# Performance work log

Measured on AMD Instinct MI355X. Metric: run time of the kernel, lower is better.

Reference implementation:

```python
import jax, jax.numpy as jnp
import numpy as np

HID = 64

def setup_inputs() -> dict:
    key = jax.random.key(0)
    ks = jax.random.split(key, 20)
    N, E, IN = 20000, 100000, 16
    s = 0.05
    return {
        "nfeat": jax.random.normal(ks[0], (N, IN), dtype=jnp.float32),
        "efeat": jax.random.normal(ks[1], (E, 5), dtype=jnp.float32),
        "src": jax.random.randint(ks[2], (E,), 0, N),
        "dst": jax.random.randint(ks[3], (E,), 0, N),
        "lin0_w": jax.random.normal(ks[4], (IN, HID)) * s,
        "lin0_b": jax.random.normal(ks[5], (HID,)) * s,
        "e1_w": jax.random.normal(ks[6], (5, 128)) * s,
        "e1_b": jax.random.normal(ks[7], (128,)) * s,
        "e2_w": jax.random.normal(ks[8], (128, HID * HID)) * s,
        "e2_b": jax.random.normal(ks[9], (HID * HID,)) * s,
        "conv_bias": jax.random.normal(ks[10], (HID,)) * s,
        "gru_w_ih": jax.random.normal(ks[11], (HID, 3 * HID)) * s,
        "gru_w_hh": jax.random.normal(ks[12], (HID, 3 * HID)) * s,
        "gru_b_ih": jax.random.normal(ks[13], (3 * HID,)) * s,
        "gru_b_hh": jax.random.normal(ks[14], (3 * HID,)) * s,
        "lstm_w_ih": jax.random.normal(ks[15], (2 * HID, 4 * HID)) * s,
        "lstm_w_hh": jax.random.normal(ks[16], (HID, 4 * HID)) * s,
        "lstm_b_ih": jax.random.normal(ks[17], (4 * HID,)) * s,
        "lstm_b_hh": jax.random.normal(ks[18], (4 * HID,)) * s,
    }


def _forward(nfeat, efeat, src, dst, lin0_w, lin0_b, e1_w, e1_b, e2_w, e2_b,
             conv_bias, gru_w_ih, gru_w_hh, gru_b_ih, gru_b_hh,
             lstm_w_ih, lstm_w_hh, lstm_b_ih, lstm_b_hh):
    N = nfeat.shape[0]
    E = efeat.shape[0]
    # lin0 + relu
    out = jax.nn.relu(nfeat @ lin0_w + lin0_b)          # [N, H]
    h = out                                             # GRU hidden state
    # edge MLP -> per-edge weight matrix [E, H, H] (in, out); efeat is fixed across rounds
    w_e = (jax.nn.relu(efeat @ e1_w + e1_b) @ e2_w + e2_b).reshape(E, HID, HID)
    # mean-aggregation denominator (in-degree, clamped like DGL mean over nonempty)
    deg = jax.ops.segment_sum(jnp.ones((E,), out.dtype), dst, num_segments=N)
    denom = jnp.maximum(deg, 1.0)[:, None]
    for _ in range(3):
        msg = jnp.einsum('ei,eio->eo', out[src], w_e)   # edge-conditioned matmul
        agg = jax.ops.segment_sum(msg, dst, num_segments=N) / denom
        m = jax.nn.relu(agg + conv_bias)                # NNConv output + relu
        # GRU cell (torch gate order: r, z, n)
        gi = m @ gru_w_ih + gru_b_ih
        gh = h @ gru_w_hh + gru_b_hh
        ir, iz, inn = jnp.split(gi, 3, axis=-1)
        hr, hz, hn = jnp.split(gh, 3, axis=-1)
        r = jax.nn.sigmoid(ir + hr)
        z = jax.nn.sigmoid(iz + hz)
        n = jnp.tanh(inn + r * hn)
        h = (1.0 - z) * n + z * h
        out = h
    # Set2Set pooling (single graph), LSTM gate order: i, f, g, o
    q_star = jnp.zeros((1, 2 * HID), out.dtype)
    hl = jnp.zeros((1, HID), out.dtype)
    cl = jnp.zeros((1, HID), out.dtype)
    for _ in range(3):
        gates = q_star @ lstm_w_ih + lstm_b_ih + hl @ lstm_w_hh + lstm_b_hh
        i_g, f_g, g_g, o_g = jnp.split(gates, 4, axis=-1)
        cl = jax.nn.sigmoid(f_g) * cl + jax.nn.sigmoid(i_g) * jnp.tanh(g_g)
        hl = jax.nn.sigmoid(o_g) * jnp.tanh(cl)
        q = hl                                          # [1, H]
        e = jnp.sum(out * q, axis=-1)                   # [N]
        alpha = jax.nn.softmax(e)
        readout = jnp.sum(alpha[:, None] * out, axis=0, keepdims=True)  # [1, H]
        q_star = jnp.concatenate([q, readout], axis=1)
    return q_star, out


def reference(nfeat, efeat, src, dst, lin0_w, lin0_b, e1_w, e1_b, e2_w, e2_b,
              conv_bias, gru_w_ih, gru_w_hh, gru_b_ih, gru_b_hh,
              lstm_w_ih, lstm_w_hh, lstm_b_ih, lstm_b_hh):
    return _forward(nfeat, efeat, src, dst, lin0_w, lin0_b, e1_w, e1_b, e2_w,
                    e2_b, conv_bias, gru_w_ih, gru_w_hh, gru_b_ih, gru_b_hh,
                    lstm_w_ih, lstm_w_hh, lstm_b_ih, lstm_b_hh)
```

## Files before the change

kernel.cpp:

```cpp
#include <hip/hip_runtime.h>

#define NN 20000
#define NE 100000
#define EPAD 100096
#define INF 16
#define HID 64

typedef __attribute__((ext_vector_type(8))) short short8;
typedef __attribute__((ext_vector_type(4))) float f32x4;

#define QS   0
#define SHL  128
#define SCL  192
#define SQ   256
#define SSW  324
#define SRD  384

__device__ inline float bf2f(unsigned short u) {
    union { unsigned u32; float f; } c; c.u32 = ((unsigned)u) << 16; return c.f;
}
__device__ inline unsigned short f2b(float f) {
    union { float f; unsigned u; } c; c.f = f;
    unsigned u = c.u;
    unsigned r = u + 0x7fffu + ((u >> 16) & 1u);
    return (unsigned short)(r >> 16);
}
__device__ inline float sigm(float x) { return 1.f / (1.f + expf(-x)); }
__device__ inline short8 s8zero() {
    short8 v;
    #pragma unroll
    for (int z = 0; z < 8; ++z) v[z] = 0;
    return v;
}
__device__ inline void gload_lds16(const void* g, void* l) {
    __builtin_amdgcn_global_load_lds(
        (const __attribute__((address_space(1))) unsigned*)g,
        (__attribute__((address_space(3))) unsigned*)l, 16, 0, 0);
}

__global__ void k_sentinel(float* out) { out[0] = 12345.0f; }

__global__ __launch_bounds__(256) void k_lin0(const float* __restrict__ nfeat,
        const float* __restrict__ w, const float* __restrict__ b,
        float* __restrict__ X, unsigned short* __restrict__ Xb) {
    int t = blockIdx.x * 256 + threadIdx.x;
    int n = t >> 6, o = t & 63;
    float acc = b[o];
    #pragma unroll
    for (int i = 0; i < INF; ++i) acc += nfeat[n * INF + i] * w[i * HID + o];
    float v = fmaxf(acc, 0.f);
    X[t] = v;
    Xb[t] = f2b(v);
}

__global__ void k_count(const int* __restrict__ dst, int* __restrict__ cnt, int E) {
    int e = blockIdx.x * blockDim.x + threadIdx.x;
    if (e < E) atomicAdd(&cnt[dst[e]], 1);
}

__global__ void k_scan(const int* __restrict__ cnt, int* __restrict__ istart) {
    __shared__ int ps[1024];
    int t = threadIdx.x;
    const int CH = (NN + 1023) / 1024;
    int lo = t * CH, hi = (lo + CH < NN) ? lo + CH : NN;
    if (lo > NN) lo = NN;
    if (hi < lo) hi = lo;
    int s = 0;
    for (int i = lo; i < hi; ++i) s += cnt[i];
    ps[t] = s;
    __syncthreads();
    for (int off = 1; off < 1024; off <<= 1) {
        int v = (t >= off) ? ps[t - off] : 0;
        __syncthreads();
        ps[t] += v;
        __syncthreads();
    }
    int run = ps[t] - s;
    for (int i = lo; i < hi; ++i) { istart[i] = run; run += cnt[i]; }
    if (t == 1023) istart[NN] = run;
}

__global__ void k_scatter(const int* __restrict__ src, const int* __restrict__ dst,
        const int* __restrict__ istart, int* __restrict__ cnt2,
        int* __restrict__ ssrc, int* __restrict__ sdst, int* __restrict__ spos, int E) {
    int e = blockIdx.x * blockDim.x + threadIdx.x;
    if (e >= E) return;
    int d = dst[e];
    int p = istart[d] + atomicAdd(&cnt2[d], 1);
    ssrc[p] = src[e];
    sdst[p] = d;
    spos[e] = p;
}

__global__ __launch_bounds__(256) void k_e1(const float* __restrict__ efeat,
        const float* __restrict__ w, const float* __restrict__ b,
        const int* __restrict__ spos, unsigned short* __restrict__ h1b) {
    int t = blockIdx.x * 256 + threadIdx.x;
    int e = t >> 7, k = t & 127;
    float acc = b[k];
    #pragma unroll
    for (int i = 0; i < 5; ++i) acc += efeat[e * 5 + i] * w[i * 128 + k];
    h1b[(size_t)spos[e] * 128 + k] = f2b(fmaxf(acc, 0.f));
}

__global__ __launch_bounds__(256) void k_tr(const float* __restrict__ w2,
        unsigned short* __restrict__ w2t) {
    __shared__ float t[128][65];
    int tid = threadIdx.x;
    int og0 = blockIdx.x * 64;
    for (int v = tid; v < 2048; v += 256) {
        int k = v >> 4, c4 = (v & 15) << 2;
        float4 val = *reinterpret_cast<const float4*>(&w2[(size_t)k * 4096 + og0 + c4]);
        t[k][c4 + 0] = val.x; t[k][c4 + 1] = val.y;
        t[k][c4 + 2] = val.z; t[k][c4 + 3] = val.w;
    }
    __syncthreads();
    int ogl = tid >> 2;
    int k0 = (tid & 3) * 32;
    unsigned short buf[32];
    #pragma unroll
    for (int j = 0; j < 32; ++j) buf[j] = f2b(t[k0 + j][ogl]);
    size_t base = (size_t)(og0 + ogl) * 128;
    #pragma unroll
    for (int q = 0; q < 4; ++q) {
        int s = (tid & 3) * 4 + q;
        int pos = (s ^ (ogl & 7)) * 8;
        short8 pv;
        #pragma unroll
        for (int z = 0; z < 8; ++z) pv[z] = buf[q * 8 + z];
        *reinterpret_cast<short8*>(&w2t[base + pos]) = pv;
    }
}

__global__ void k_prep(const float* __restrict__ e2b, unsigned short* __restrict__ b2t) {
    int t = blockIdx.x * 256 + threadIdx.x;
    int o = t >> 6, i = t & 63;
    b2t[o * 64 + i] = f2b(e2b[i * 64 + o]);
}

__global__ __launch_bounds__(256, 4) void k_msg(
        const unsigned short* __restrict__ Xb,
        const unsigned short* __restrict__ h1b,
        const unsigned short* __restrict__ w2t,
        const unsigned short* __restrict__ b2t,
        const int* __restrict__ ssrc, const int* __restrict__ sdst,
        const int* __restrict__ istart, float* __restrict__ agg) {
    __shared__ __align__(16) char smem[35328];
    unsigned short* xeb = (unsigned short*)(smem + 16384);
    int* sdst_s         = (int*)(smem + 34816);
    const int tid = threadIdx.x;
    const int e0 = blockIdx.x * 128;
    const int y  = blockIdx.y;
    const int w = tid >> 6, l = tid & 63;
    const int wo_l = (w >> 1) * 16;
    const int weh  = (w & 1) * 64;
    const int l15 = l & 15, lh = l >> 4;

    for (int v = tid; v < 1024; v += 256) {
        int row = v >> 3, c8 = (v & 7) << 3;
        int ee = e0 + row;
        short8 val = s8zero();
        if (ee < NE)
            val = *reinterpret_cast<const short8*>(&Xb[(size_t)ssrc[ee] * 64 + c8]);
        *reinterpret_cast<short8*>(&xeb[row * 72 + c8]) = val;
    }
    if (tid < 128) {
        int ee = e0 + tid;
        sdst_s[tid] = (ee < NE) ? sdst[ee] : NN;
    }

    {
        const char* g0 = (const char*)w2t + (size_t)y * 8192;
        gload_lds16(g0 + w * 2048 + l * 16, smem + w * 2048);
        gload_lds16(g0 + w * 2048 + 1024 + l * 16, smem + w * 2048 + 1024);
    }

    short8 bfr[4][4];
    #pragma unroll
    for (int ef = 0; ef < 4; ++ef) {
        const unsigned short* hp = &h1b[(size_t)(e0 + weh + ef * 16 + l15) * 128 + lh * 8];
        #pragma unroll
        for (int ks = 0; ks < 4; ++ks)
            bfr[ef][ks] = *reinterpret_cast<const short8*>(hp + ks * 32);
    }

    f32x4 acc[4];
    #pragma unroll
    for (int ef = 0; ef < 4; ++ef) acc[ef] = f32x4{0.f, 0.f, 0.f, 0.f};
    const f32x4 zero = f32x4{0.f, 0.f, 0.f, 0.f};

    __syncthreads();

    const int r = wo_l + l15;
    const int sw = r & 7;
    int cur = 0;
    #pragma unroll 1
    for (int i = 0; i < 64; ++i) {
        if (i < 63) {
            const char* g = (const char*)w2t + (size_t)(i + 1) * 16384 + (size_t)y * 8192;
            char* dbase = smem + (cur ^ 1) * 8192;
            gload_lds16(g + w * 2048 + l * 16, dbase + w * 2048);
            gload_lds16(g + w * 2048 + 1024 + l * 16, dbase + w * 2048 + 1024);
        }
        float xv[4];
        #pragma unroll
        for (int ef = 0; ef < 4; ++ef)
            xv[ef] = bf2f(xeb[(weh + ef * 16 + l15) * 72 + i]);

        const unsigned short* rb = (const unsigned short*)(smem + cur * 8192) + r * 128;
        short8 a0 = *reinterpret_cast<const short8*>(&rb[((0 + lh) ^ sw) << 3]);
        short8 a1 = *reinterpret_cast<const short8*>(&rb[((4 + lh) ^ sw) << 3]);
        short8 a2 = *reinterpret_cast<const short8*>(&rb[((8 + lh) ^ sw) << 3]);
        short8 a3 = *reinterpret_cast<const short8*>(&rb[((12 + lh) ^ sw) << 3]);
        #pragma unroll
        for (int ef = 0; ef < 4; ++ef) {
            f32x4 t = __builtin_amdgcn_mfma_f32_16x16x32_bf16(a0, bfr[ef][0], zero, 0, 0, 0);
            t = __builtin_amdgcn_mfma_f32_16x16x32_bf16(a1, bfr[ef][1], t, 0, 0, 0);
            t = __builtin_amdgcn_mfma_f32_16x16x32_bf16(a2, bfr[ef][2], t, 0, 0, 0);
            t = __builtin_amdgcn_mfma_f32_16x16x32_bf16(a3, bfr[ef][3], t, 0, 0, 0);
            #pragma unroll
            for (int rr = 0; rr < 4; ++rr) acc[ef][rr] += xv[ef] * t[rr];
        }
        __syncthreads();
        cur ^= 1;
    }

    {
        const unsigned short* bp = &b2t[(y * 32 + r) * 64 + lh * 8];
        short8 ba0 = *reinterpret_cast<const short8*>(bp);
        short8 ba1 = *reinterpret_cast<const short8*>(bp + 32);
        #pragma unroll
        for (int ef = 0; ef < 4; ++ef) {
            int e = e0 + weh + ef * 16 + l15;
            int es = (e < NE) ? ssrc[e] : 0;
            const unsigned short* xp = &Xb[(size_t)es * 64 + lh * 8];
            short8 x0 = *reinterpret_cast<const short8*>(xp);
            short8 x1 = *reinterpret_cast<const short8*>(xp + 32);
            f32x4 tb = __builtin_amdgcn_mfma_f32_16x16x32_bf16(ba0, x0, zero, 0, 0, 0);
            tb = __builtin_amdgcn_mfma_f32_16x16x32_bf16(ba1, x1, tb, 0, 0, 0);
            #pragma unroll
            for (int rr = 0; rr < 4; ++rr) acc[ef][rr] += tb[rr];
        }
    }

    __syncthreads();
    float* msgL = (float*)smem;
    #pragma unroll
    for (int ef = 0; ef < 4; ++ef)
        #pragma unroll
        for (int rr = 0; rr < 4; ++rr)
            msgL[(weh + ef * 16 + l15) * 33 + (wo_l + lh * 4 + rr)] = acc[ef][rr];
    __syncthreads();

    if (tid < 128) {
        int o = tid & 31, win = tid >> 5;
        int base = win << 5;
        int lo = e0 + base, hi = lo + 32;
        int cn = -1; float s = 0.f;
        for (int e2 = base; e2 < base + 32; ++e2) {
            int n = sdst_s[e2];
            if (n != cn) {
                if (cn >= 0 && cn < NN) {
                    int st = istart[cn], en = istart[cn + 1];
                    if (st >= lo && en <= hi) agg[(size_t)cn * 64 + y * 32 + o] = s;
                    else atomicAdd(&agg[(size_t)cn * 64 + y * 32 + o], s);
                }
                cn = n; s = 0.f;
            }
            s += msgL[e2 * 33 + o];
        }
        if (cn >= 0 && cn < NN) {
            int st = istart[cn], en = istart[cn + 1];
            if (st >= lo && en <= hi) agg[(size_t)cn * 64 + y * 32 + o] = s;
            else atomicAdd(&agg[(size_t)cn * 64 + y * 32 + o], s);
        }
    }
}

__global__ __launch_bounds__(256) void k_gru(const float* __restrict__ agg,
        const int* __restrict__ istart, const float* __restrict__ cbias,
        const float* __restrict__ wih, const float* __restrict__ whh,
        const float* __restrict__ bih, const float* __restrict__ bhh,
        float* __restrict__ X, unsigned short* __restrict__ Xb) {
    __shared__ float ms[16][65], hs[16][65];
    int tid = threadIdx.x;
    int l = tid & 63, g = tid >> 6;
    int nb = blockIdx.x * 16;
    for (int v = tid; v < 1024; v += 256) {
        int row = v >> 6, c = v & 63;
        int n = nb + row;
        float dv = fmaxf((float)(istart[n + 1] - istart[n]), 1.f);
        ms[row][c] = fmaxf(agg[(size_t)n * 64 + c] / dv + cbias[c], 0.f);
        hs[row][c] = X[(size_t)n * 64 + c];
    }
    __syncthreads();
    float gr[4], gz[4], gn[4], hr[4], hz[4], hn[4];
    float b0 = bih[l], b1 = bih[64 + l], b2 = bih[128 + l];
    float c0 = bhh[l], c1 = bhh[64 + l], c2 = bhh[128 + l];
    #pragma unroll
    for (int j = 0; j < 4; ++j) {
        gr[j] = b0; gz[j] = b1; gn[j] = b2;
        hr[j] = c0; hz[j] = c1; hn[j] = c2;
    }
    #pragma unroll 4
    for (int i = 0; i < 64; ++i) {
        float wr = wih[i * 192 + l], wz = wih[i * 192 + 64 + l], wn = wih[i * 192 + 128 + l];
        float vr = whh[i * 192 + l], vz = whh[i * 192 + 64 + l], vn = whh[i * 192 + 128 + l];
        #pragma unroll
        for (int j = 0; j < 4; ++j) {
            float mi = ms[g * 4 + j][i], hi = hs[g * 4 + j][i];
            gr[j] += mi * wr; gz[j] += mi * wz; gn[j] += mi * wn;
            hr[j] += hi * vr; hz[j] += hi * vz; hn[j] += hi * vn;
        }
    }
    #pragma unroll
    for (int j = 0; j < 4; ++j) {
        int n = nb + g * 4 + j;
        float h = hs[g * 4 + j][l];
        float r = sigm(gr[j] + hr[j]);
        float z = sigm(gz[j] + hz[j]);
        float nn2 = tanhf(gn[j] + r * hn[j]);
        float newh = (1.f - z) * nn2 + z * h;
        X[(size_t)n * 64 + l] = newh;
        Xb[(size_t)n * 64 + l] = f2b(newh);
    }
}

__global__ void k_lstm(const float* __restrict__ wih, const float* __restrict__ whh,
        const float* __restrict__ bih, const float* __restrict__ bhh,
        float* __restrict__ scal, int it) {
    __shared__ float qs[128];
    __shared__ float g[256];
    int t = threadIdx.x;
    if (t < 128) {
        float v = 0.f;
        if (it > 0)
            v = (t < 64) ? scal[SQ + t]
                         : scal[SRD + (it - 1) * 64 + (t - 64)] / scal[SSW + (it - 1)];
        qs[t] = v;
    }
    __syncthreads();
    float acc = bih[t] + bhh[t];
    for (int i = 0; i < 128; ++i) acc += qs[i] * wih[i * 256 + t];
    for (int i = 0; i < 64; ++i)  acc += scal[SHL + i] * whh[i * 256 + t];
    g[t] = acc;
    __syncthreads();
    if (t < 64) {
        float ig = sigm(g[t]), fg = sigm(g[64 + t]);
        float gg = tanhf(g[128 + t]), og = sigm(g[192 + t]);
        float c = fg * scal[SCL + t] + ig * gg;
        float h = og * tanhf(c);
        scal[SCL + t] = c; scal[SHL + t] = h; scal[SQ + t] = h;
    }
}

__global__ __launch_bounds__(256) void k_pool(const float* __restrict__ X,
        float* __restrict__ scal, int it) {
    __shared__ float accs[4][65];
    __shared__ float sws[4];
    int tid = threadIdx.x;
    int w = tid >> 6, l = tid & 63;
    float q = scal[SQ + l];
    int gw = blockIdx.x * 4 + w;
    float acc = 0.f, sw = 0.f;
    for (int n = gw; n < NN; n += 512) {
        float xl = X[(size_t)n * 64 + l];
        float v = xl * q;
        #pragma unroll
        for (int off = 32; off; off >>= 1) v += __shfl_xor(v, off, 64);
        float wt = expf(v);
        acc += wt * xl;
        sw += wt;
    }
    accs[w][l] = acc;
    if (l == 0) sws[w] = sw;
    __syncthreads();
    if (w == 0) {
        float a = accs[0][l] + accs[1][l] + accs[2][l] + accs[3][l];
        atomicAdd(&scal[SRD + it * 64 + l], a);
        if (l == 0) atomicAdd(&scal[SSW + it], sws[0] + sws[1] + sws[2] + sws[3]);
    }
}

__global__ void k_fin(const float* __restrict__ scal, float* __restrict__ dq) {
    int t = threadIdx.x;
    float v;
    if (t < 64) v = scal[SQ + t];
    else        v = scal[SRD + 2 * 64 + (t - 64)] / scal[SSW + 2];
    dq[t] = v;
}

extern "C" void kernel_launch(void* const* d_in, const int* in_sizes, int n_in,
                              void* d_out, int out_size, void* d_ws, size_t ws_size,
                              hipStream_t stream) {
    const float* nfeat   = (const float*)d_in[0];
    const float* efeat   = (const float*)d_in[1];
    const int*   src     = (const int*)d_in[2];
    const int*   dst     = (const int*)d_in[3];
    const float* lin0_w  = (const float*)d_in[4];
    const float* lin0_b  = (const float*)d_in[5];
    const float* e1_w    = (const float*)d_in[6];
    const float* e1_b    = (const float*)d_in[7];
    const float* e2_w    = (const float*)d_in[8];
    const float* e2_b    = (const float*)d_in[9];
    const float* conv_b  = (const float*)d_in[10];
    const float* gwih    = (const float*)d_in[11];
    const float* gwhh    = (const float*)d_in[12];
    const float* gbih    = (const float*)d_in[13];
    const float* gbhh    = (const float*)d_in[14];
    const float* lwih    = (const float*)d_in[15];
    const float* lwhh    = (const float*)d_in[16];
    const float* lbih    = (const float*)d_in[17];
    const float* lbhh    = (const float*)d_in[18];

    const int N = NN, E = NE;

    size_t off = 0;
    auto take = [&](size_t bytes) { size_t o = off; off = (off + bytes + 255) & ~(size_t)255; return o; };
    size_t oX    = take((size_t)N * 64 * 4);
    size_t oAgg  = take((size_t)N * 64 * 4);
    size_t oScal = take(4096);
    size_t oH1   = take((size_t)EPAD * 128 * 2);
    size_t oW2T  = take((size_t)4096 * 128 * 2);
    size_t oXb   = take((size_t)N * 64 * 2);
    size_t oB2T  = take((size_t)64 * 64 * 2);
    size_t oIst  = take((size_t)(N + 1) * 4);
    size_t oIc1  = take((size_t)N * 4);
    size_t oIc2  = take((size_t)N * 4);
    size_t oSs   = take((size_t)E * 4);
    size_t oSd   = take((size_t)E * 4);
    size_t oSp   = take((size_t)E * 4);
    size_t needed = off;

    float* outp = (float*)d_out;
    if (ws_size < needed) {
        k_sentinel<<<1, 1, 0, stream>>>(outp);
        return;
    }

    char* wsb = (char*)d_ws;
    float* X    = (float*)(wsb + oX);
    float* agg  = (float*)(wsb + oAgg);
    float* scal = (float*)(wsb + oScal);
    unsigned short* h1b = (unsigned short*)(wsb + oH1);
    unsigned short* w2t = (unsigned short*)(wsb + oW2T);
    unsigned short* Xb  = (unsigned short*)(wsb + oXb);
    unsigned short* b2t = (unsigned short*)(wsb + oB2T);
    int* istart = (int*)(wsb + oIst);
    int* icnt   = (int*)(wsb + oIc1);
    int* icnt2  = (int*)(wsb + oIc2);
    int* ssrc   = (int*)(wsb + oSs);
    int* sdst   = (int*)(wsb + oSd);
    int* spos   = (int*)(wsb + oSp);

    hipMemsetAsync(scal, 0, 4096, stream);
    hipMemsetAsync(icnt, 0, (size_t)N * 4, stream);
    hipMemsetAsync(icnt2, 0, (size_t)N * 4, stream);
    hipMemsetAsync(h1b + (size_t)E * 128, 0, (size_t)(EPAD - E) * 128 * 2, stream);

    k_lin0<<<(N * HID) / 256, 256, 0, stream>>>(nfeat, lin0_w, lin0_b, X, Xb);
    k_count<<<(E + 255) / 256, 256, 0, stream>>>(dst, icnt, E);
    k_scan<<<1, 1024, 0, stream>>>(icnt, istart);
    k_scatter<<<(E + 255) / 256, 256, 0, stream>>>(src, dst, istart, icnt2, ssrc, sdst, spos, E);
    k_e1<<<(E * 128) / 256, 256, 0, stream>>>(efeat, e1_w, e1_b, spos, h1b);
    k_tr<<<64, 256, 0, stream>>>(e2_w, w2t);
    k_prep<<<16, 256, 0, stream>>>(e2_b, b2t);

    for (int r = 0; r < 3; ++r) {
        hipMemsetAsync(agg, 0, (size_t)N * 64 * 4, stream);
        k_msg<<<dim3(EPAD / 128, 2), 256, 0, stream>>>(Xb, h1b, w2t, b2t, ssrc, sdst, istart, agg);
        k_gru<<<N / 16, 256, 0, stream>>>(agg, istart, conv_b, gwih, gwhh, gbih, gbhh, X, Xb);
    }

    for (int it = 0; it < 3; ++it) {
        k_lstm<<<1, 256, 0, stream>>>(lwih, lwhh, lbih, lbhh, scal, it);
        k_pool<<<128, 256, 0, stream>>>(X, scal, it);
    }
    k_fin<<<1, 128, 0, stream>>>(scal, outp);

    hipMemcpyAsync(outp + 128, X, (size_t)N * 64 * 4, hipMemcpyDeviceToDevice, stream);
}
```

Before: 596.1 us.

## Deepen k_msg weight prefetch to 4-stage ring and double GRU rows per block

The message kernel's LDS staging of the edge-MLP weight slices moves from double buffering to a four-slot ring with a two-iteration prefetch distance. Explicit vmcnt waits plus a raw s_barrier replace the full __syncthreads, so loads can stay in flight across iterations. LDS grows to about 51KB and the occupancy hint drops from 4 to 3 blocks per CU. The GRU kernel also processes 32 nodes per block instead of 16, reusing each weight load across more rows at the cost of more registers.

```diff
diff --git a/kernel.cpp b/kernel.cpp
--- a/kernel.cpp
+++ b/kernel.cpp
@@ -138,16 +138,16 @@
     b2t[o * 64 + i] = f2b(e2b[i * 64 + o]);
 }
 
-__global__ __launch_bounds__(256, 4) void k_msg(
+__global__ __launch_bounds__(256, 3) void k_msg(
         const unsigned short* __restrict__ Xb,
         const unsigned short* __restrict__ h1b,
         const unsigned short* __restrict__ w2t,
         const unsigned short* __restrict__ b2t,
         const int* __restrict__ ssrc, const int* __restrict__ sdst,
         const int* __restrict__ istart, float* __restrict__ agg) {
-    __shared__ __align__(16) char smem[35328];
-    unsigned short* xeb = (unsigned short*)(smem + 16384);
-    int* sdst_s         = (int*)(smem + 34816);
+    __shared__ __align__(16) char smem[51712];
+    unsigned short* xeb = (unsigned short*)(smem + 32768);
+    int* sdst_s         = (int*)(smem + 51200);
     const int tid = threadIdx.x;
     const int e0 = blockIdx.x * 128;
     const int y  = blockIdx.y;
@@ -169,12 +169,6 @@
         sdst_s[tid] = (ee < NE) ? sdst[ee] : NN;
     }
 
-    {
-        const char* g0 = (const char*)w2t + (size_t)y * 8192;
-        gload_lds16(g0 + w * 2048 + l * 16, smem + w * 2048);
-        gload_lds16(g0 + w * 2048 + 1024 + l * 16, smem + w * 2048 + 1024);
-    }
-
     short8 bfr[4][4];
     #pragma unroll
     for (int ef = 0; ef < 4; ++ef) {
@@ -191,23 +185,27 @@
 
     __syncthreads();
 
+    #pragma unroll
+    for (int pb = 0; pb < 2; ++pb) {
+        const char* g = (const char*)w2t + (size_t)pb * 16384 + (size_t)y * 8192 + w * 2048;
+        char* d = smem + pb * 8192 + w * 2048;
+        gload_lds16(g + l * 16, d);
+        gload_lds16(g + 1024 + l * 16, d + 1024);
+    }
+    asm volatile("s_waitcnt vmcnt(2)" ::: "memory");
+    __builtin_amdgcn_sched_barrier(0);
+    __builtin_amdgcn_s_barrier();
+
     const int r = wo_l + l15;
     const int sw = r & 7;
-    int cur = 0;
     #pragma unroll 1
     for (int i = 0; i < 64; ++i) {
-        if (i < 63) {
-            const char* g = (const char*)w2t + (size_t)(i + 1) * 16384 + (size_t)y * 8192;
-            char* dbase = smem + (cur ^ 1) * 8192;
-            gload_lds16(g + w * 2048 + l * 16, dbase + w * 2048);
-            gload_lds16(g + w * 2048 + 1024 + l * 16, dbase + w * 2048 + 1024);
-        }
         float xv[4];
         #pragma unroll
         for (int ef = 0; ef < 4; ++ef)
             xv[ef] = bf2f(xeb[(weh + ef * 16 + l15) * 72 + i]);
 
-        const unsigned short* rb = (const unsigned short*)(smem + cur * 8192) + r * 128;
+        const unsigned short* rb = (const unsigned short*)(smem + (i & 3) * 8192) + r * 128;
         short8 a0 = *reinterpret_cast<const short8*>(&rb[((0 + lh) ^ sw) << 3]);
         short8 a1 = *reinterpret_cast<const short8*>(&rb[((4 + lh) ^ sw) << 3]);
         short8 a2 = *reinterpret_cast<const short8*>(&rb[((8 + lh) ^ sw) << 3]);
@@ -221,8 +219,18 @@
             #pragma unroll
             for (int rr = 0; rr < 4; ++rr) acc[ef][rr] += xv[ef] * t[rr];
         }
-        __syncthreads();
-        cur ^= 1;
+
+        if (i < 62) {
+            const char* g = (const char*)w2t + (size_t)(i + 2) * 16384 + (size_t)y * 8192 + w * 2048;
+            char* d = smem + ((i + 2) & 3) * 8192 + w * 2048;
+            gload_lds16(g + l * 16, d);
+            gload_lds16(g + 1024 + l * 16, d + 1024);
+            asm volatile("s_waitcnt vmcnt(2)" ::: "memory");
+        } else if (i == 62) {
+            asm volatile("s_waitcnt vmcnt(0)" ::: "memory");
+        }
+        __builtin_amdgcn_sched_barrier(0);
+        __builtin_amdgcn_s_barrier();
     }
 
     {
@@ -282,11 +290,11 @@
         const float* __restrict__ wih, const float* __restrict__ whh,
         const float* __restrict__ bih, const float* __restrict__ bhh,
         float* __restrict__ X, unsigned short* __restrict__ Xb) {
-    __shared__ float ms[16][65], hs[16][65];
+    __shared__ float ms[32][65], hs[32][65];
     int tid = threadIdx.x;
     int l = tid & 63, g = tid >> 6;
-    int nb = blockIdx.x * 16;
-    for (int v = tid; v < 1024; v += 256) {
+    int nb = blockIdx.x * 32;
+    for (int v = tid; v < 2048; v += 256) {
         int row = v >> 6, c = v & 63;
         int n = nb + row;
         float dv = fmaxf((float)(istart[n + 1] - istart[n]), 1.f);
@@ -294,29 +302,29 @@
         hs[row][c] = X[(size_t)n * 64 + c];
     }
     __syncthreads();
-    float gr[4], gz[4], gn[4], hr[4], hz[4], hn[4];
+    float gr[8], gz[8], gn[8], hr[8], hz[8], hn[8];
     float b0 = bih[l], b1 = bih[64 + l], b2 = bih[128 + l];
     float c0 = bhh[l], c1 = bhh[64 + l], c2 = bhh[128 + l];
     #pragma unroll
-    for (int j = 0; j < 4; ++j) {
+    for (int j = 0; j < 8; ++j) {
         gr[j] = b0; gz[j] = b1; gn[j] = b2;
         hr[j] = c0; hz[j] = c1; hn[j] = c2;
     }
-    #pragma unroll 4
+    #pragma unroll 2
     for (int i = 0; i < 64; ++i) {
         float wr = wih[i * 192 + l], wz = wih[i * 192 + 64 + l], wn = wih[i * 192 + 128 + l];
         float vr = whh[i * 192 + l], vz = whh[i * 192 + 64 + l], vn = whh[i * 192 + 128 + l];
         #pragma unroll
-        for (int j = 0; j < 4; ++j) {
-            float mi = ms[g * 4 + j][i], hi = hs[g * 4 + j][i];
+        for (int j = 0; j < 8; ++j) {
+            float mi = ms[g * 8 + j][i], hi = hs[g * 8 + j][i];
             gr[j] += mi * wr; gz[j] += mi * wz; gn[j] += mi * wn;
             hr[j] += hi * vr; hz[j] += hi * vz; hn[j] += hi * vn;
         }
     }
     #pragma unroll
-    for (int j = 0; j < 4; ++j) {
-        int n = nb + g * 4 + j;
-        float h = hs[g * 4 + j][l];
+    for (int j = 0; j < 8; ++j) {
+        int n = nb + g * 8 + j;
+        float h = hs[g * 8 + j][l];
         float r = sigm(gr[j] + hr[j]);
         float z = sigm(gz[j] + hz[j]);
         float nn2 = tanhf(gn[j] + r * hn[j]);
@@ -469,7 +477,7 @@
     for (int r = 0; r < 3; ++r) {
         hipMemsetAsync(agg, 0, (size_t)N * 64 * 4, stream);
         k_msg<<<dim3(EPAD / 128, 2), 256, 0, stream>>>(Xb, h1b, w2t, b2t, ssrc, sdst, istart, agg);
-        k_gru<<<N / 16, 256, 0, stream>>>(agg, istart, conv_b, gwih, gwhh, gbih, gbhh, X, Xb);
+        k_gru<<<N / 32, 256, 0, stream>>>(agg, istart, conv_b, gwih, gwhh, gbih, gbhh, X, Xb);
     }
 
     for (int it = 0; it < 3; ++it) {
```

Result: slower. 646.4 us (+8.4%).

## Load edge-MLP weight fragments directly from global into registers, dropping LDS staging

Applied to the files above, without the earlier changes.

The message kernel stops staging each 64-row slice of the transposed edge-MLP weight through double-buffered LDS with async global-to-LDS loads and a per-iteration barrier. Each lane now reads its MFMA A-fragments straight from global memory into registers, two iterations at a time with software prefetch, and the transpose kernel writes an unswizzled layout to match. This removes 64 block barriers per block and cuts shared memory use, but adds register pressure (occupancy hint lowered from 4 to 3) and relies on L2/cache hits for the repeated weight reads, since every wave now fetches weights independently.

```diff
diff --git a/kernel.cpp b/kernel.cpp
--- a/kernel.cpp
+++ b/kernel.cpp
@@ -31,11 +31,6 @@
     #pragma unroll
     for (int z = 0; z < 8; ++z) v[z] = 0;
     return v;
-}
-__device__ inline void gload_lds16(const void* g, void* l) {
-    __builtin_amdgcn_global_load_lds(
-        (const __attribute__((address_space(1))) unsigned*)g,
-        (__attribute__((address_space(3))) unsigned*)l, 16, 0, 0);
 }
 
 __global__ void k_sentinel(float* out) { out[0] = 12345.0f; }
@@ -120,15 +115,13 @@
     unsigned short buf[32];
     #pragma unroll
     for (int j = 0; j < 32; ++j) buf[j] = f2b(t[k0 + j][ogl]);
-    size_t base = (size_t)(og0 + ogl) * 128;
+    size_t base = (size_t)(og0 + ogl) * 128 + k0;
     #pragma unroll
     for (int q = 0; q < 4; ++q) {
-        int s = (tid & 3) * 4 + q;
-        int pos = (s ^ (ogl & 7)) * 8;
         short8 pv;
         #pragma unroll
         for (int z = 0; z < 8; ++z) pv[z] = buf[q * 8 + z];
-        *reinterpret_cast<short8*>(&w2t[base + pos]) = pv;
+        *reinterpret_cast<short8*>(&w2t[base + q * 8]) = pv;
     }
 }
 
@@ -138,16 +131,16 @@
     b2t[o * 64 + i] = f2b(e2b[i * 64 + o]);
 }
 
-__global__ __launch_bounds__(256, 4) void k_msg(
+__global__ __launch_bounds__(256, 3) void k_msg(
         const unsigned short* __restrict__ Xb,
         const unsigned short* __restrict__ h1b,
         const unsigned short* __restrict__ w2t,
         const unsigned short* __restrict__ b2t,
         const int* __restrict__ ssrc, const int* __restrict__ sdst,
         const int* __restrict__ istart, float* __restrict__ agg) {
-    __shared__ __align__(16) char smem[35328];
-    unsigned short* xeb = (unsigned short*)(smem + 16384);
-    int* sdst_s         = (int*)(smem + 34816);
+    __shared__ __align__(16) char smem[18944];
+    unsigned short* xeb = (unsigned short*)smem;
+    int* sdst_s         = (int*)(smem + 18432);
     const int tid = threadIdx.x;
     const int e0 = blockIdx.x * 128;
     const int y  = blockIdx.y;
@@ -169,12 +162,6 @@
         sdst_s[tid] = (ee < NE) ? sdst[ee] : NN;
     }
 
-    {
-        const char* g0 = (const char*)w2t + (size_t)y * 8192;
-        gload_lds16(g0 + w * 2048 + l * 16, smem + w * 2048);
-        gload_lds16(g0 + w * 2048 + 1024 + l * 16, smem + w * 2048 + 1024);
-    }
-
     short8 bfr[4][4];
     #pragma unroll
     for (int ef = 0; ef < 4; ++ef) {
@@ -189,44 +176,72 @@
     for (int ef = 0; ef < 4; ++ef) acc[ef] = f32x4{0.f, 0.f, 0.f, 0.f};
     const f32x4 zero = f32x4{0.f, 0.f, 0.f, 0.f};
 
-    __syncthreads();
-
-    const int r = wo_l + l15;
-    const int sw = r & 7;
-    int cur = 0;
+    const int r = y * 32 + wo_l + l15;
+    const char* wp = (const char*)w2t + (size_t)r * 256 + lh * 16;
+
+    __syncthreads();
+
+    short8 aA0, aA1, aA2, aA3, aB0, aB1, aB2, aB3;
+    {
+        const char* p0 = wp;
+        aA0 = *reinterpret_cast<const short8*>(p0);
+        aA1 = *reinterpret_cast<const short8*>(p0 + 64);
+        aA2 = *reinterpret_cast<const short8*>(p0 + 128);
+        aA3 = *reinterpret_cast<const short8*>(p0 + 192);
+        const char* p1 = wp + 16384;
+        aB0 = *reinterpret_cast<const short8*>(p1);
+        aB1 = *reinterpret_cast<const short8*>(p1 + 64);
+        aB2 = *reinterpret_cast<const short8*>(p1 + 128);
+        aB3 = *reinterpret_cast<const short8*>(p1 + 192);
+    }
+
     #pragma unroll 1
-    for (int i = 0; i < 64; ++i) {
-        if (i < 63) {
-            const char* g = (const char*)w2t + (size_t)(i + 1) * 16384 + (size_t)y * 8192;
-            char* dbase = smem + (cur ^ 1) * 8192;
-            gload_lds16(g + w * 2048 + l * 16, dbase + w * 2048);
-            gload_lds16(g + w * 2048 + 1024 + l * 16, dbase + w * 2048 + 1024);
-        }
-        float xv[4];
-        #pragma unroll
-        for (int ef = 0; ef < 4; ++ef)
-            xv[ef] = bf2f(xeb[(weh + ef * 16 + l15) * 72 + i]);
-
-        const unsigned short* rb = (const unsigned short*)(smem + cur * 8192) + r * 128;
-        short8 a0 = *reinterpret_cast<const short8*>(&rb[((0 + lh) ^ sw) << 3]);
-        short8 a1 = *reinterpret_cast<const short8*>(&rb[((4 + lh) ^ sw) << 3]);
-        short8 a2 = *reinterpret_cast<const short8*>(&rb[((8 + lh) ^ sw) << 3]);
-        short8 a3 = *reinterpret_cast<const short8*>(&rb[((12 + lh) ^ sw) << 3]);
+    for (int ii = 0; ii < 32; ++ii) {
+        const int i0 = ii * 2;
+        float xv0[4], xv1[4];
         #pragma unroll
         for (int ef = 0; ef < 4; ++ef) {
-            f32x4 t = __builtin_amdgcn_mfma_f32_16x16x32_bf16(a0, bfr[ef][0], zero, 0, 0, 0);
-            t = __builtin_amdgcn_mfma_f32_16x16x32_bf16(a1, bfr[ef][1], t, 0, 0, 0);
-            t = __builtin_amdgcn_mfma_f32_16x16x32_bf16(a2, bfr[ef][2], t, 0, 0, 0);
-            t = __builtin_amdgcn_mfma_f32_16x16x32_bf16(a3, bfr[ef][3], t, 0, 0, 0);
+            unsigned v = *reinterpret_cast<const unsigned*>(
+                &xeb[(weh + ef * 16 + l15) * 72 + i0]);
+            xv0[ef] = bf2f((unsigned short)(v & 0xffffu));
+            xv1[ef] = bf2f((unsigned short)(v >> 16));
+        }
+        #pragma unroll
+        for (int ef = 0; ef < 4; ++ef) {
+            f32x4 t = __builtin_amdgcn_mfma_f32_16x16x32_bf16(aA0, bfr[ef][0], zero, 0, 0, 0);
+            t = __builtin_amdgcn_mfma_f32_16x16x32_bf16(aA1, bfr[ef][1], t, 0, 0, 0);
+            t = __builtin_amdgcn_mfma_f32_16x16x32_bf16(aA2, bfr[ef][2], t, 0, 0, 0);
+            t = __builtin_amdgcn_mfma_f32_16x16x32_bf16(aA3, bfr[ef][3], t, 0, 0, 0);
             #pragma unroll
-            for (int rr = 0; rr < 4; ++rr) acc[ef][rr] += xv[ef] * t[rr];
-        }
-        __syncthreads();
-        cur ^= 1;
+            for (int rr = 0; rr < 4; ++rr) acc[ef][rr] += xv0[ef] * t[rr];
+        }
+        if (ii < 31) {
+            const char* p = wp + (size_t)(i0 + 2) * 16384;
+            aA0 = *reinterpret_cast<const short8*>(p);
+            aA1 = *reinterpret_cast<const short8*>(p + 64);
+            aA2 = *reinterpret_cast<const short8*>(p + 128);
+            aA3 = *reinterpret_cast<const short8*>(p + 192);
+        }
+        #pragma unroll
+        for (int ef = 0; ef < 4; ++ef) {
+            f32x4 t = __builtin_amdgcn_mfma_f32_16x16x32_bf16(aB0, bfr[ef][0], zero, 0, 0, 0);
+            t = __builtin_amdgcn_mfma_f32_16x16x32_bf16(aB1, bfr[ef][1], t, 0, 0, 0);
+            t = __builtin_amdgcn_mfma_f32_16x16x32_bf16(aB2, bfr[ef][2], t, 0, 0, 0);
+            t = __builtin_amdgcn_mfma_f32_16x16x32_bf16(aB3, bfr[ef][3], t, 0, 0, 0);
+            #pragma unroll
+            for (int rr = 0; rr < 4; ++rr) acc[ef][rr] += xv1[ef] * t[rr];
+        }
+        if (ii < 31) {
+            const char* p = wp + (size_t)(i0 + 3) * 16384;
+            aB0 = *reinterpret_cast<const short8*>(p);
+            aB1 = *reinterpret_cast<const short8*>(p + 64);
+            aB2 = *reinterpret_cast<const short8*>(p + 128);
+            aB3 = *reinterpret_cast<const short8*>(p + 192);
+        }
     }
 
     {
-        const unsigned short* bp = &b2t[(y * 32 + r) * 64 + lh * 8];
+        const unsigned short* bp = &b2t[r * 64 + lh * 8];
         short8 ba0 = *reinterpret_cast<const short8*>(bp);
         short8 ba1 = *reinterpret_cast<const short8*>(bp + 32);
         #pragma unroll
```

Measured after the change: 945.0 us. 1.59x slower.

## Merge k_msg output halves into one block, fuse LSTM into pool, drop final copy

Applied to the files above, without the earlier changes.

k_msg now runs one 512-thread block per 128-edge tile that covers all 64 output columns, instead of two 256-thread blocks that each covered 32. This means the per-edge h1b fragments, the gathered source features and the destination indices are loaded once rather than twice, at the cost of a larger LDS footprint per block (double-buffered weight slabs of 16 KB each) and fewer resident blocks. The LSTM cell step is folded into every k_pool block, which each recompute it redundantly, so three single-block launches disappear. The last GRU round writes the node output straight into the output buffer, which removes the trailing device-to-device memcpy.

```diff
diff --git a/kernel.cpp b/kernel.cpp
--- a/kernel.cpp
+++ b/kernel.cpp
@@ -9,12 +9,10 @@
 typedef __attribute__((ext_vector_type(8))) short short8;
 typedef __attribute__((ext_vector_type(4))) float f32x4;
 
-#define QS   0
-#define SHL  128
-#define SCL  192
-#define SQ   256
-#define SSW  324
-#define SRD  384
+#define SSW0 0
+#define SRD0 16
+#define HL0  256
+#define CL0  512
 
 __device__ inline float bf2f(unsigned short u) {
     union { unsigned u32; float f; } c; c.u32 = ((unsigned)u) << 16; return c.f;
@@ -138,25 +136,24 @@
     b2t[o * 64 + i] = f2b(e2b[i * 64 + o]);
 }
 
-__global__ __launch_bounds__(256, 4) void k_msg(
+__global__ __launch_bounds__(512, 6) void k_msg(
         const unsigned short* __restrict__ Xb,
         const unsigned short* __restrict__ h1b,
         const unsigned short* __restrict__ w2t,
         const unsigned short* __restrict__ b2t,
         const int* __restrict__ ssrc, const int* __restrict__ sdst,
         const int* __restrict__ istart, float* __restrict__ agg) {
-    __shared__ __align__(16) char smem[35328];
-    unsigned short* xeb = (unsigned short*)(smem + 16384);
-    int* sdst_s         = (int*)(smem + 34816);
+    __shared__ __align__(16) char smem[51712];
+    unsigned short* xeb = (unsigned short*)(smem + 32768);
+    int* sdst_s         = (int*)(smem + 51200);
     const int tid = threadIdx.x;
     const int e0 = blockIdx.x * 128;
-    const int y  = blockIdx.y;
     const int w = tid >> 6, l = tid & 63;
-    const int wo_l = (w >> 1) * 16;
-    const int weh  = (w & 1) * 64;
+    const int wo  = (w >> 1) * 16;
+    const int weh = (w & 1) * 64;
     const int l15 = l & 15, lh = l >> 4;
 
-    for (int v = tid; v < 1024; v += 256) {
+    for (int v = tid; v < 1024; v += 512) {
         int row = v >> 3, c8 = (v & 7) << 3;
         int ee = e0 + row;
         short8 val = s8zero();
@@ -170,9 +167,9 @@
     }
 
     {
-        const char* g0 = (const char*)w2t + (size_t)y * 8192;
-        gload_lds16(g0 + w * 2048 + l * 16, smem + w * 2048);
-        gload_lds16(g0 + w * 2048 + 1024 + l * 16, smem + w * 2048 + 1024);
+        const char* g0 = (const char*)w2t + w * 2048;
+        gload_lds16(g0 + l * 16, smem + w * 2048);
+        gload_lds16(g0 + 1024 + l * 16, smem + w * 2048 + 1024);
     }
 
     short8 bfr[4][4];
@@ -191,23 +188,23 @@
 
     __syncthreads();
 
-    const int r = wo_l + l15;
+    const int r = wo + l15;
     const int sw = r & 7;
     int cur = 0;
     #pragma unroll 1
     for (int i = 0; i < 64; ++i) {
         if (i < 63) {
-            const char* g = (const char*)w2t + (size_t)(i + 1) * 16384 + (size_t)y * 8192;
-            char* dbase = smem + (cur ^ 1) * 8192;
-            gload_lds16(g + w * 2048 + l * 16, dbase + w * 2048);
-            gload_lds16(g + w * 2048 + 1024 + l * 16, dbase + w * 2048 + 1024);
+            const char* g = (const char*)w2t + (size_t)(i + 1) * 16384 + w * 2048;
+            char* dbase = smem + (cur ^ 1) * 16384 + w * 2048;
+            gload_lds16(g + l * 16, dbase);
+            gload_lds16(g + 1024 + l * 16, dbase + 1024);
         }
         float xv[4];
         #pragma unroll
         for (int ef = 0; ef < 4; ++ef)
             xv[ef] = bf2f(xeb[(weh + ef * 16 + l15) * 72 + i]);
 
-        const unsigned short* rb = (const unsigned short*)(smem + cur * 8192) + r * 128;
+        const unsigned short* rb = (const unsigned short*)(smem + cur * 16384) + r * 128;
         short8 a0 = *reinterpret_cast<const short8*>(&rb[((0 + lh) ^ sw) << 3]);
         short8 a1 = *reinterpret_cast<const short8*>(&rb[((4 + lh) ^ sw) << 3]);
         short8 a2 = *reinterpret_cast<const short8*>(&rb[((8 + lh) ^ sw) << 3]);
@@ -226,7 +223,7 @@
     }
 
     {
-        const unsigned short* bp = &b2t[(y * 32 + r) * 64 + lh * 8];
+        const unsigned short* bp = &b2t[r * 64 + lh * 8];
         short8 ba0 = *reinterpret_cast<const short8*>(bp);
         short8 ba1 = *reinterpret_cast<const short8*>(bp + 32);
         #pragma unroll
@@ -249,11 +246,11 @@
     for (int ef = 0; ef < 4; ++ef)
         #pragma unroll
         for (int rr = 0; rr < 4; ++rr)
-            msgL[(weh + ef * 16 + l15) * 33 + (wo_l + lh * 4 + rr)] = acc[ef][rr];
-    __syncthreads();
-
-    if (tid < 128) {
-        int o = tid & 31, win = tid >> 5;
+            msgL[(weh + ef * 16 + l15) * 65 + (wo + lh * 4 + rr)] = acc[ef][rr];
+    __syncthreads();
+
+    if (tid < 256) {
+        int o = tid & 63, win = tid >> 6;
         int base = win << 5;
         int lo = e0 + base, hi = lo + 32;
         int cn = -1; float s = 0.f;
@@ -262,17 +259,17 @@
             if (n != cn) {
                 if (cn >= 0 && cn < NN) {
                     int st = istart[cn], en = istart[cn + 1];
-                    if (st >= lo && en <= hi) agg[(size_t)cn * 64 + y * 32 + o] = s;
-                    else atomicAdd(&agg[(size_t)cn * 64 + y * 32 + o], s);
+                    if (st >= lo && en <= hi) agg[(size_t)cn * 64 + o] = s;
+                    else atomicAdd(&agg[(size_t)cn * 64 + o], s);
                 }
                 cn = n; s = 0.f;
             }
-            s += msgL[e2 * 33 + o];
+            s += msgL[e2 * 65 + o];
         }
         if (cn >= 0 && cn < NN) {
             int st = istart[cn], en = istart[cn + 1];
-            if (st >= lo && en <= hi) agg[(size_t)cn * 64 + y * 32 + o] = s;
-            else atomicAdd(&agg[(size_t)cn * 64 + y * 32 + o], s);
+            if (st >= lo && en <= hi) agg[(size_t)cn * 64 + o] = s;
+            else atomicAdd(&agg[(size_t)cn * 64 + o], s);
         }
     }
 }
@@ -281,7 +278,8 @@
         const int* __restrict__ istart, const float* __restrict__ cbias,
         const float* __restrict__ wih, const float* __restrict__ whh,
         const float* __restrict__ bih, const float* __restrict__ bhh,
-        float* __restrict__ X, unsigned short* __restrict__ Xb) {
+        float* __restrict__ X, unsigned short* __restrict__ Xb,
+        float* __restrict__ Xout) {
     __shared__ float ms[16][65], hs[16][65];
     int tid = threadIdx.x;
     int l = tid & 63, g = tid >> 6;
@@ -323,70 +321,70 @@
         float newh = (1.f - z) * nn2 + z * h;
         X[(size_t)n * 64 + l] = newh;
         Xb[(size_t)n * 64 + l] = f2b(newh);
-    }
-}
-
-__global__ void k_lstm(const float* __restrict__ wih, const float* __restrict__ whh,
-        const float* __restrict__ bih, const float* __restrict__ bhh,
+        if (Xout) Xout[(size_t)n * 64 + l] = newh;
+    }
+}
+
+__global__ __launch_bounds__(256) void k_pool(const float* __restrict__ X,
+        const float* __restrict__ lwih, const float* __restrict__ lwhh,
+        const float* __restrict__ lbih, const float* __restrict__ lbhh,
         float* __restrict__ scal, int it) {
-    __shared__ float qs[128];
-    __shared__ float g[256];
+    __shared__ float qsin[128];
+    __shared__ float gg[256];
+    __shared__ float qsh[64];
+    __shared__ float accs[4][65];
+    __shared__ float sws[4];
     int t = threadIdx.x;
     if (t < 128) {
-        float v = 0.f;
-        if (it > 0)
-            v = (t < 64) ? scal[SQ + t]
-                         : scal[SRD + (it - 1) * 64 + (t - 64)] / scal[SSW + (it - 1)];
-        qs[t] = v;
-    }
-    __syncthreads();
-    float acc = bih[t] + bhh[t];
-    for (int i = 0; i < 128; ++i) acc += qs[i] * wih[i * 256 + t];
-    for (int i = 0; i < 64; ++i)  acc += scal[SHL + i] * whh[i * 256 + t];
-    g[t] = acc;
+        float v;
+        if (t < 64) v = scal[HL0 + it * 64 + t];
+        else        v = (it > 0) ? scal[SRD0 + (it - 1) * 64 + (t - 64)] / scal[SSW0 + it - 1] : 0.f;
+        qsin[t] = v;
+    }
+    __syncthreads();
+    float acc = lbih[t] + lbhh[t];
+    for (int i = 0; i < 128; ++i) acc += qsin[i] * lwih[i * 256 + t];
+    for (int i = 0; i < 64; ++i)  acc += qsin[i] * lwhh[i * 256 + t];
+    gg[t] = acc;
     __syncthreads();
     if (t < 64) {
-        float ig = sigm(g[t]), fg = sigm(g[64 + t]);
-        float gg = tanhf(g[128 + t]), og = sigm(g[192 + t]);
-        float c = fg * scal[SCL + t] + ig * gg;
-        float h = og * tanhf(c);
-        scal[SCL + t] = c; scal[SHL + t] = h; scal[SQ + t] = h;
-    }
-}
-
-__global__ __launch_bounds__(256) void k_pool(const float* __restrict__ X,
-        float* __restrict__ scal, int it) {
-    __shared__ float accs[4][65];
-    __shared__ float sws[4];
-    int tid = threadIdx.x;
-    int w = tid >> 6, l = tid & 63;
-    float q = scal[SQ + l];
+        float ig = sigm(gg[t]), fg = sigm(gg[64 + t]);
+        float g2 = tanhf(gg[128 + t]), og = sigm(gg[192 + t]);
+        float cl = fg * scal[CL0 + it * 64 + t] + ig * g2;
+        float hl = og * tanhf(cl);
+        scal[CL0 + (it + 1) * 64 + t] = cl;
+        scal[HL0 + (it + 1) * 64 + t] = hl;
+        qsh[t] = hl;
+    }
+    __syncthreads();
+    int w = t >> 6, l = t & 63;
+    float q = qsh[l];
     int gw = blockIdx.x * 4 + w;
-    float acc = 0.f, sw = 0.f;
+    float pacc = 0.f, sw = 0.f;
     for (int n = gw; n < NN; n += 512) {
         float xl = X[(size_t)n * 64 + l];
         float v = xl * q;
         #pragma unroll
         for (int off = 32; off; off >>= 1) v += __shfl_xor(v, off, 64);
         float wt = expf(v);
-        acc += wt * xl;
+        pacc += wt * xl;
         sw += wt;
     }
-    accs[w][l] = acc;
+    accs[w][l] = pacc;
     if (l == 0) sws[w] = sw;
     __syncthreads();
     if (w == 0) {
         float a = accs[0][l] + accs[1][l] + accs[2][l] + accs[3][l];
-        atomicAdd(&scal[SRD + it * 64 + l], a);
-        if (l == 0) atomicAdd(&scal[SSW + it], sws[0] + sws[1] + sws[2] + sws[3]);
+        atomicAdd(&scal[SRD0 + it * 64 + l], a);
+        if (l == 0) atomicAdd(&scal[SSW0 + it], sws[0] + sws[1] + sws[2] + sws[3]);
     }
 }
 
 __global__ void k_fin(const float* __restrict__ scal, float* __restrict__ dq) {
     int t = threadIdx.x;
     float v;
-    if (t < 64) v = scal[SQ + t];
-    else        v = scal[SRD + 2 * 64 + (t - 64)] / scal[SSW + 2];
+    if (t < 64) v = scal[HL0 + 3 * 64 + t];
+    else        v = scal[SRD0 + 2 * 64 + (t - 64)] / scal[SSW0 + 2];
     dq[t] = v;
 }
 
@@ -468,15 +466,13 @@
 
     for (int r = 0; r < 3; ++r) {
         hipMemsetAsync(agg, 0, (size_t)N * 64 * 4, stream);
-        k_msg<<<dim3(EPAD / 128, 2), 256, 0, stream>>>(Xb, h1b, w2t, b2t, ssrc, sdst, istart, agg);
-        k_gru<<<N / 16, 256, 0, stream>>>(agg, istart, conv_b, gwih, gwhh, gbih, gbhh, X, Xb);
+        k_msg<<<EPAD / 128, 512, 0, stream>>>(Xb, h1b, w2t, b2t, ssrc, sdst, istart, agg);
+        k_gru<<<N / 16, 256, 0, stream>>>(agg, istart, conv_b, gwih, gwhh, gbih, gbhh,
+                                          X, Xb, (r == 2) ? (outp + 128) : nullptr);
     }
 
     for (int it = 0; it < 3; ++it) {
-        k_lstm<<<1, 256, 0, stream>>>(lwih, lwhh, lbih, lbhh, scal, it);
-        k_pool<<<128, 256, 0, stream>>>(X, scal, it);
+        k_pool<<<128, 256, 0, stream>>>(X, lwih, lwhh, lbih, lbhh, scal, it);
     }
     k_fin<<<1, 128, 0, stream>>>(scal, outp);
-
-    hipMemcpyAsync(outp + 128, X, (size_t)N * 64 * 4, hipMemcpyDeviceToDevice, stream);
-}
+}
```

New measurement: 2.063 ms. 3.46x slower.
